# Kernel optimization log

Hardware: AMD Instinct MI355X
Metric: run time of the kernel (lower is better)

## Reference

```python
import jax, jax.numpy as jnp
import numpy as np

NUM_HEADS = 8


def _conv1x1(x, W, b):
    # 1x1 conv == per-pixel linear: x [N,C,H,W], W [O,C], b [O]
    return jnp.einsum('nchw,oc->nohw', x, W) + b[None, :, None, None]


def setup_inputs() -> dict:
    key = jax.random.key(0)
    ks = jax.random.split(key, 10)
    C = 512
    s = 1.0 / np.sqrt(C)  # keep pre-softmax logits in a sane range
    return {
        'x': jax.random.normal(ks[0], (2, C, 64, 64), dtype=jnp.float32),
        'Wq': jax.random.normal(ks[1], (C, C), dtype=jnp.float32) * s,
        'bq': jax.random.normal(ks[2], (C,), dtype=jnp.float32) * 0.01,
        'Wk': jax.random.normal(ks[3], (C, C), dtype=jnp.float32) * s,
        'bk': jax.random.normal(ks[4], (C,), dtype=jnp.float32) * 0.01,
        'Wv': jax.random.normal(ks[5], (C, C), dtype=jnp.float32) * s,
        'bv': jax.random.normal(ks[6], (C,), dtype=jnp.float32) * 0.01,
        'Wo': jax.random.normal(ks[7], (C, C), dtype=jnp.float32) * s,
        'bo': jax.random.normal(ks[8], (C,), dtype=jnp.float32) * 0.01,
        'gamma': jax.random.normal(ks[9], (1,), dtype=jnp.float32),
    }


def reference(x, Wq, bq, Wk, bk, Wv, bv, Wo, bo, gamma):
    N, C, H, W = x.shape
    nh = NUM_HEADS
    hd = C // nh
    S = H * W
    scale = 1.0 / (hd ** 0.5)
    # Projections via 1x1 conv, then split heads over flattened spatial tokens
    Q = _conv1x1(x, Wq, bq).reshape(N, nh, hd, S).transpose(0, 1, 3, 2)  # [N,h,S,d]
    K = _conv1x1(x, Wk, bk).reshape(N, nh, hd, S)                         # [N,h,d,S]
    V = _conv1x1(x, Wv, bv).reshape(N, nh, hd, S).transpose(0, 1, 3, 2)  # [N,h,S,d]
    attn = jax.nn.softmax(jnp.einsum('nhsd,nhdt->nhst', Q, K) * scale, axis=-1)
    out = jnp.einsum('nhst,nhtd->nhsd', attn, V)                          # [N,h,S,d]
    out = out.transpose(0, 1, 3, 2).reshape(N, C, H, W)
    out = _conv1x1(out, Wo, bo)
    return gamma[0] * out + x
```

## Files before the change

kernel.cpp:

```cpp
#include <hip/hip_runtime.h>
#include <hip/hip_bf16.h>

typedef __attribute__((ext_vector_type(4))) float f32x4;
typedef __attribute__((ext_vector_type(16))) float f32x16;
typedef __attribute__((ext_vector_type(8))) short s16x8;
typedef __attribute__((ext_vector_type(4))) unsigned short us16x4;
typedef __attribute__((ext_vector_type(4))) unsigned int u32x4;

#define C_DIM 512
#define S_DIM 4096
#define NB 2
#define NH 8
#define HD 64

#define QSCALE 0.1803368801111244f

__device__ __forceinline__ unsigned short f2bf(float f) {
    union { float f; unsigned u; } v; v.f = f;
    unsigned r = v.u + 0x7FFFu + ((v.u >> 16) & 1u);
    return (unsigned short)(r >> 16);
}

__device__ __forceinline__ float dev_exp2(float x) {
    float r;
    asm("v_exp_f32 %0, %1" : "=v"(r) : "v"(x));
    return r;
}

__device__ __forceinline__ unsigned cvt_pk_bf16(float lo, float hi) {
    unsigned r;
    asm("v_cvt_pk_bf16_f32 %0, %1, %2" : "=v"(r) : "v"(lo), "v"(hi));
    return r;
}

__device__ __forceinline__ void lane_swap(unsigned& a, unsigned& b) {
    asm("v_permlane32_swap_b32 %0, %1" : "+v"(a), "+v"(b));
}

__device__ __forceinline__ void gload_lds16(const void* g, void* l) {
    __builtin_amdgcn_global_load_lds(
        (const __attribute__((address_space(1))) void*)g,
        (__attribute__((address_space(3))) void*)l, 16, 0, 0);
}

__global__ __launch_bounds__(256) void wconv_kernel(
    const float* __restrict__ Wq, const float* __restrict__ Wk,
    const float* __restrict__ Wv, const float* __restrict__ Wo,
    unsigned short* __restrict__ Wb) {
    int i = blockIdx.x * 256 + threadIdx.x;
    int y = blockIdx.y;
    const float* src = (y == 0) ? Wq : (y == 1) ? Wk : (y == 2) ? Wv : Wo;
    Wb[(size_t)y * 262144 + i] = f2bf(src[i]);
}

__global__ __launch_bounds__(256) void xpose_kernel(
    const float* __restrict__ x, unsigned short* __restrict__ Xt) {
    __shared__ float tile[32][132];
    int n = blockIdx.z;
    int s0 = blockIdx.x * 128;
    int c0 = blockIdx.y * 32;
    int t = threadIdx.x;
    int cr = t >> 3, scol = (t & 7) * 16;
    const float* src = &x[((size_t)n * C_DIM + c0 + cr) * S_DIM + s0 + scol];
#pragma unroll
    for (int i = 0; i < 4; ++i)
        *(f32x4*)&tile[cr][scol + i * 4] = *(const f32x4*)&src[i * 4];
    __syncthreads();
    int sr = t >> 1, ch = (t & 1) * 16;
    unsigned short* dst = &Xt[((size_t)n * S_DIM + s0 + sr) * C_DIM + c0 + ch];
#pragma unroll
    for (int half = 0; half < 2; ++half) {
        s16x8 pk;
#pragma unroll
        for (int j = 0; j < 8; ++j)
            pk[j] = (short)f2bf(tile[ch + half * 8 + j][sr]);
        *(s16x8*)&dst[half * 8] = pk;
    }
}

__global__ __launch_bounds__(256) void qkv_gemm_kernel(
    const unsigned short* __restrict__ Wb, const unsigned short* __restrict__ Xt,
    const float* __restrict__ bq, const float* __restrict__ bk, const float* __restrict__ bv,
    unsigned short* __restrict__ Qt, unsigned short* __restrict__ Kt,
    unsigned short* __restrict__ Vb) {
    __shared__ unsigned short As[128 * 64];
    __shared__ unsigned short Bs[128 * 64];
    int w = blockIdx.z >> 1;
    int n = blockIdx.z & 1;
    const unsigned short* A = Wb + (size_t)w * 262144;
    const unsigned short* B = Xt + (size_t)n * S_DIM * C_DIM;
    int tid = threadIdx.x;
    int wid = tid >> 6, lane = tid & 63;
    int wm = wid >> 1, wn = wid & 1;
    int lr = lane & 15, lq = lane >> 4;
    int bm = blockIdx.y * 128, bt = blockIdx.x * 128;
    int r_in = lane >> 3, c8 = (lane & 7) * 8;

    f32x4 zero = {0.f, 0.f, 0.f, 0.f};
    f32x4 acc[4][4];
#pragma unroll
    for (int i = 0; i < 4; ++i)
#pragma unroll
        for (int j = 0; j < 4; ++j) acc[i][j] = zero;

    for (int ks = 0; ks < 8; ++ks) {
#pragma unroll
        for (int q = 0; q < 4; ++q) {
            int row = wid * 32 + q * 8;
            gload_lds16(A + (size_t)(bm + row + r_in) * C_DIM + ks * 64 + c8, &As[row * 64]);
            gload_lds16(B + (size_t)(bt + row + r_in) * C_DIM + ks * 64 + c8, &Bs[row * 64]);
        }
        __syncthreads();
#pragma unroll
        for (int kk = 0; kk < 2; ++kk) {
            s16x8 af[4], bf[4];
#pragma unroll
            for (int i = 0; i < 4; ++i)
                af[i] = *(const s16x8*)&As[(wm * 64 + i * 16 + lr) * 64 + kk * 32 + lq * 8];
#pragma unroll
            for (int j = 0; j < 4; ++j)
                bf[j] = *(const s16x8*)&Bs[(wn * 64 + j * 16 + lr) * 64 + kk * 32 + lq * 8];
#pragma unroll
            for (int i = 0; i < 4; ++i)
#pragma unroll
                for (int j = 0; j < 4; ++j)
                    acc[i][j] = __builtin_amdgcn_mfma_f32_16x16x32_bf16(af[i], bf[j], acc[i][j], 0, 0, 0);
        }
        __syncthreads();
    }

    const float* bias = (w == 0) ? bq : (w == 1) ? bk : bv;
#pragma unroll
    for (int i = 0; i < 4; ++i) {
        int obase = bm + wm * 64 + i * 16 + lq * 4;
#pragma unroll
        for (int j = 0; j < 4; ++j) {
            int t = bt + wn * 64 + j * 16 + lr;
            if (w == 0) {
                us16x4 pk;
#pragma unroll
                for (int r = 0; r < 4; ++r)
                    pk[r] = f2bf((acc[i][j][r] + bias[obase + r]) * QSCALE);
                int h = obase >> 6, d = obase & 63;
                *(us16x4*)&Qt[(((size_t)(n * NH + h) * S_DIM) + t) * HD + d] = pk;
            } else if (w == 1) {
                us16x4 pk;
#pragma unroll
                for (int r = 0; r < 4; ++r) pk[r] = f2bf(acc[i][j][r] + bias[obase + r]);
                int h = obase >> 6, d = obase & 63;
                *(us16x4*)&Kt[(((size_t)(n * NH + h) * S_DIM) + t) * HD + d] = pk;
            } else {
#pragma unroll
                for (int r = 0; r < 4; ++r) {
                    int o = obase + r;
                    Vb[((size_t)(n * C_DIM + o)) * S_DIM + t] = f2bf(acc[i][j][r] + bias[o]);
                }
            }
        }
    }
}

__global__ __launch_bounds__(256) void attn_kernel(
    const unsigned short* __restrict__ Qt, const unsigned short* __restrict__ Kt,
    const unsigned short* __restrict__ Vb, unsigned short* __restrict__ Ot) {
    __shared__ unsigned short Ks[64 * 64];
    __shared__ unsigned short Vs[64 * 64];
    int tid = threadIdx.x, wid = tid >> 6, lane = tid & 63;
    int l31 = lane & 31, hi = lane >> 5;
    int radj = (l31 & 7) ^ ((l31 >> 3) & 3);

    int bidl = blockIdx.x;
    int swz = (bidl & 7) * 64 + (bidl >> 3);
    int nh = swz >> 5;
    int qb = swz & 31;
    int n = nh >> 3, h = nh & 7;
    int qrow0 = qb * 128 + wid * 32;

    const unsigned short* Qh = Qt + (size_t)nh * S_DIM * HD;
    const unsigned short* Kh = Kt + (size_t)nh * S_DIM * HD;
    const unsigned short* Vh = Vb + ((size_t)(n * C_DIM + h * HD)) * S_DIM;

    s16x8 qf[4];
#pragma unroll
    for (int st = 0; st < 4; ++st)
        qf[st] = *(const s16x8*)&Qh[((size_t)(qrow0 + l31)) * HD + st * 16 + hi * 8];

    s16x8 ones;
#pragma unroll
    for (int r = 0; r < 8; ++r) ones[r] = (short)0x3F80;

    f32x16 Oacc[2], Lacc;
#pragma unroll
    for (int jm = 0; jm < 2; ++jm)
#pragma unroll
        for (int r = 0; r < 16; ++r) Oacc[jm][r] = 0.f;
#pragma unroll
    for (int r = 0; r < 16; ++r) Lacc[r] = 0.f;

    int srow0 = tid >> 3, sslot = tid & 7;
    int wslot = (sslot ^ (srow0 & 7) ^ ((srow0 >> 3) & 3)) * 8;

    s16x8 kreg[2], vreg[2];
#pragma unroll
    for (int q = 0; q < 2; ++q) {
        int row = srow0 + q * 32;
        kreg[q] = *(const s16x8*)&Kh[((size_t)row) * HD + sslot * 8];
        vreg[q] = *(const s16x8*)&Vh[((size_t)row) * S_DIM + sslot * 8];
    }

    for (int kt = 0; kt < 64; ++kt) {
#pragma unroll
        for (int q = 0; q < 2; ++q) {
            int row = srow0 + q * 32;
            *(s16x8*)&Ks[row * 64 + wslot] = kreg[q];
            *(s16x8*)&Vs[row * 64 + wslot] = vreg[q];
        }
        __syncthreads();
        if (kt < 63) {
#pragma unroll
            for (int q = 0; q < 2; ++q) {
                int row = srow0 + q * 32;
                kreg[q] = *(const s16x8*)&Kh[((size_t)((kt + 1) * 64 + row)) * HD + sslot * 8];
                vreg[q] = *(const s16x8*)&Vh[((size_t)row) * S_DIM + (kt + 1) * 64 + sslot * 8];
            }
        }

        f32x16 s_[2];
#pragma unroll
        for (int jm = 0; jm < 2; ++jm) {
#pragma unroll
            for (int r = 0; r < 16; ++r) s_[jm][r] = 0.f;
            int arow = jm * 32 + l31;
#pragma unroll
            for (int st = 0; st < 4; ++st) {
                s16x8 kf = *(const s16x8*)&Ks[arow * 64 + ((2 * st + hi) ^ radj) * 8];
                s_[jm] = __builtin_amdgcn_mfma_f32_32x32x16_bf16(kf, qf[st], s_[jm], 0, 0, 0);
            }
        }

        s16x8 pf[2][2];
#pragma unroll
        for (int jm = 0; jm < 2; ++jm) {
            unsigned pk0 = cvt_pk_bf16(dev_exp2(s_[jm][0]),  dev_exp2(s_[jm][1]));
            unsigned pk1 = cvt_pk_bf16(dev_exp2(s_[jm][2]),  dev_exp2(s_[jm][3]));
            unsigned pk2 = cvt_pk_bf16(dev_exp2(s_[jm][4]),  dev_exp2(s_[jm][5]));
            unsigned pk3 = cvt_pk_bf16(dev_exp2(s_[jm][6]),  dev_exp2(s_[jm][7]));
            unsigned pk4 = cvt_pk_bf16(dev_exp2(s_[jm][8]),  dev_exp2(s_[jm][9]));
            unsigned pk5 = cvt_pk_bf16(dev_exp2(s_[jm][10]), dev_exp2(s_[jm][11]));
            unsigned pk6 = cvt_pk_bf16(dev_exp2(s_[jm][12]), dev_exp2(s_[jm][13]));
            unsigned pk7 = cvt_pk_bf16(dev_exp2(s_[jm][14]), dev_exp2(s_[jm][15]));
            lane_swap(pk2, pk0);
            lane_swap(pk3, pk1);
            lane_swap(pk6, pk4);
            lane_swap(pk7, pk5);
            u32x4 w0 = {pk0, pk1, pk2, pk3};
            u32x4 w1 = {pk4, pk5, pk6, pk7};
            pf[jm][0] = __builtin_bit_cast(s16x8, w0);
            pf[jm][1] = __builtin_bit_cast(s16x8, w1);
        }

#pragma unroll
        for (int jm = 0; jm < 2; ++jm)
#pragma unroll
            for (int st = 0; st < 2; ++st)
                Lacc = __builtin_amdgcn_mfma_f32_32x32x16_bf16(ones, pf[jm][st], Lacc, 0, 0, 0);

#pragma unroll
        for (int jm2 = 0; jm2 < 2; ++jm2) {
            int vrow = jm2 * 32 + l31;
#pragma unroll
            for (int jm = 0; jm < 2; ++jm)
#pragma unroll
                for (int st = 0; st < 2; ++st) {
                    s16x8 vf = *(const s16x8*)&Vs[vrow * 64 + ((jm * 4 + st * 2 + hi) ^ radj) * 8];
                    Oacc[jm2] = __builtin_amdgcn_mfma_f32_32x32x16_bf16(vf, pf[jm][st], Oacc[jm2], 0, 0, 0);
                }
        }
        __syncthreads();
    }

    float inv = 1.f / Lacc[0];
    int token = qrow0 + l31;
    unsigned short* orow = Ot + ((size_t)n * S_DIM + token) * C_DIM + h * HD;
#pragma unroll
    for (int jm2 = 0; jm2 < 2; ++jm2)
#pragma unroll
        for (int rq = 0; rq < 4; ++rq) {
            int d = jm2 * 32 + 8 * rq + 4 * hi;
            us16x4 pk;
#pragma unroll
            for (int r = 0; r < 4; ++r) pk[r] = f2bf(Oacc[jm2][rq * 4 + r] * inv);
            *(us16x4*)&orow[d] = pk;
        }
}

__global__ __launch_bounds__(256) void out_gemm_kernel(
    const unsigned short* __restrict__ Wb, const unsigned short* __restrict__ Ot,
    const float* __restrict__ bo, const float* __restrict__ gamma,
    const float* __restrict__ xin, float* __restrict__ out) {
    __shared__ unsigned short As[128 * 64];
    __shared__ unsigned short Bs[128 * 64];
    int n = blockIdx.z;
    const unsigned short* A = Wb + (size_t)3 * 262144;
    const unsigned short* B = Ot + (size_t)n * S_DIM * C_DIM;
    int tid = threadIdx.x;
    int wid = tid >> 6, lane = tid & 63;
    int wm = wid >> 1, wn = wid & 1;
    int lr = lane & 15, lq = lane >> 4;
    int bm = blockIdx.y * 128, bt = blockIdx.x * 128;
    int r_in = lane >> 3, c8 = (lane & 7) * 8;

    f32x4 zero = {0.f, 0.f, 0.f, 0.f};
    f32x4 acc[4][4];
#pragma unroll
    for (int i = 0; i < 4; ++i)
#pragma unroll
        for (int j = 0; j < 4; ++j) acc[i][j] = zero;

    for (int ks = 0; ks < 8; ++ks) {
#pragma unroll
        for (int q = 0; q < 4; ++q) {
            int row = wid * 32 + q * 8;
            gload_lds16(A + (size_t)(bm + row + r_in) * C_DIM + ks * 64 + c8, &As[row * 64]);
            gload_lds16(B + (size_t)(bt + row + r_in) * C_DIM + ks * 64 + c8, &Bs[row * 64]);
        }
        __syncthreads();
#pragma unroll
        for (int kk = 0; kk < 2; ++kk) {
            s16x8 af[4], bf[4];
#pragma unroll
            for (int i = 0; i < 4; ++i)
                af[i] = *(const s16x8*)&As[(wm * 64 + i * 16 + lr) * 64 + kk * 32 + lq * 8];
#pragma unroll
            for (int j = 0; j < 4; ++j)
                bf[j] = *(const s16x8*)&Bs[(wn * 64 + j * 16 + lr) * 64 + kk * 32 + lq * 8];
#pragma unroll
            for (int i = 0; i < 4; ++i)
#pragma unroll
                for (int j = 0; j < 4; ++j)
                    acc[i][j] = __builtin_amdgcn_mfma_f32_16x16x32_bf16(af[i], bf[j], acc[i][j], 0, 0, 0);
        }
        __syncthreads();
    }

    float g = gamma[0];
#pragma unroll
    for (int i = 0; i < 4; ++i) {
        int obase = bm + wm * 64 + i * 16 + lq * 4;
#pragma unroll
        for (int j = 0; j < 4; ++j) {
            int t = bt + wn * 64 + j * 16 + lr;
#pragma unroll
            for (int r = 0; r < 4; ++r) {
                int o = obase + r;
                size_t idx = ((size_t)(n * C_DIM + o)) * S_DIM + t;
                out[idx] = g * (acc[i][j][r] + bo[o]) + xin[idx];
            }
        }
    }
}

extern "C" void kernel_launch(void* const* d_in, const int* in_sizes, int n_in,
                              void* d_out, int out_size, void* d_ws, size_t ws_size,
                              hipStream_t stream) {
    const float* x  = (const float*)d_in[0];
    const float* Wq = (const float*)d_in[1];
    const float* bq = (const float*)d_in[2];
    const float* Wk = (const float*)d_in[3];
    const float* bk = (const float*)d_in[4];
    const float* Wv = (const float*)d_in[5];
    const float* bv = (const float*)d_in[6];
    const float* Wo = (const float*)d_in[7];
    const float* bo = (const float*)d_in[8];
    const float* gamma = (const float*)d_in[9];
    float* out = (float*)d_out;

    char* ws = (char*)d_ws;
    unsigned short* Wb = (unsigned short*)ws;
    unsigned short* Xt = (unsigned short*)(ws + ((size_t)2  << 20));
    unsigned short* Qt = (unsigned short*)(ws + ((size_t)10 << 20));
    unsigned short* Kt = (unsigned short*)(ws + ((size_t)18 << 20));
    unsigned short* Vb = (unsigned short*)(ws + ((size_t)26 << 20));
    unsigned short* Ot = (unsigned short*)(ws + ((size_t)34 << 20));

    wconv_kernel<<<dim3(1024, 4), 256, 0, stream>>>(Wq, Wk, Wv, Wo, Wb);
    xpose_kernel<<<dim3(32, 16, 2), 256, 0, stream>>>(x, Xt);
    qkv_gemm_kernel<<<dim3(32, 4, 6), 256, 0, stream>>>(Wb, Xt, bq, bk, bv, Qt, Kt, Vb);
    attn_kernel<<<512, 256, 0, stream>>>(Qt, Kt, Vb, Ot);
    out_gemm_kernel<<<dim3(32, 4, 2), 256, 0, stream>>>(Wb, Ot, bo, gamma, x, out);
}
```

Measured before the change: 147.1 us.

## Double-buffer K/V tiles in attention with direct global-to-LDS loads

The attention kernel previously prefetched the next K/V tile into registers and then wrote it to a single shared-memory buffer, with barriers around each write. It now keeps two LDS buffers per tensor and issues direct global-to-LDS loads for tile kt+1 while computing on tile kt. The XOR swizzle moves from the LDS write address to the global source address. This is meant to remove the register staging and ds_write traffic and to overlap loads with MFMA work. In exchange it doubles LDS use per block, which can lower occupancy, and it relies on the barrier correctly waiting for the async LDS loads.

```diff
diff --git a/kernel.cpp b/kernel.cpp
--- a/kernel.cpp
+++ b/kernel.cpp
@@ -163,8 +163,8 @@
 __global__ __launch_bounds__(256) void attn_kernel(
     const unsigned short* __restrict__ Qt, const unsigned short* __restrict__ Kt,
     const unsigned short* __restrict__ Vb, unsigned short* __restrict__ Ot) {
-    __shared__ unsigned short Ks[64 * 64];
-    __shared__ unsigned short Vs[64 * 64];
+    __shared__ unsigned short Ks[2][64 * 64];
+    __shared__ unsigned short Vs[2][64 * 64];
     int tid = threadIdx.x, wid = tid >> 6, lane = tid & 63;
     int l31 = lane & 31, hi = lane >> 5;
     int radj = (l31 & 7) ^ ((l31 >> 3) & 3);
@@ -197,33 +197,29 @@
 #pragma unroll
     for (int r = 0; r < 16; ++r) Lacc[r] = 0.f;
 
-    int srow0 = tid >> 3, sslot = tid & 7;
-    int wslot = (sslot ^ (srow0 & 7) ^ ((srow0 >> 3) & 3)) * 8;
-
-    s16x8 kreg[2], vreg[2];
-#pragma unroll
-    for (int q = 0; q < 2; ++q) {
-        int row = srow0 + q * 32;
-        kreg[q] = *(const s16x8*)&Kh[((size_t)row) * HD + sslot * 8];
-        vreg[q] = *(const s16x8*)&Vh[((size_t)row) * S_DIM + sslot * 8];
-    }
+    int lr8 = lane >> 3, pslot = lane & 7;
+    int row_a = wid * 16 + lr8;
+    int row_b = row_a + 8;
+    int sca = (pslot ^ (row_a & 7) ^ ((row_a >> 3) & 3)) * 8;
+    int scb = (pslot ^ (row_b & 7) ^ ((row_b >> 3) & 3)) * 8;
+    int rb_a = (wid * 16) * 64;
+    int rb_b = (wid * 16 + 8) * 64;
+
+#define STAGE_KV(buf, kt_) {                                                        \
+        const unsigned short* kb_ = Kh + ((size_t)((kt_) * 64)) * HD;               \
+        gload_lds16(kb_ + (size_t)row_a * HD + sca, &Ks[buf][rb_a]);                \
+        gload_lds16(kb_ + (size_t)row_b * HD + scb, &Ks[buf][rb_b]);                \
+        const unsigned short* vb_ = Vh + (kt_) * 64;                                \
+        gload_lds16(vb_ + (size_t)row_a * S_DIM + sca, &Vs[buf][rb_a]);             \
+        gload_lds16(vb_ + (size_t)row_b * S_DIM + scb, &Vs[buf][rb_b]);             \
+    }
+
+    STAGE_KV(0, 0);
+    __syncthreads();
 
     for (int kt = 0; kt < 64; ++kt) {
-#pragma unroll
-        for (int q = 0; q < 2; ++q) {
-            int row = srow0 + q * 32;
-            *(s16x8*)&Ks[row * 64 + wslot] = kreg[q];
-            *(s16x8*)&Vs[row * 64 + wslot] = vreg[q];
-        }
-        __syncthreads();
-        if (kt < 63) {
-#pragma unroll
-            for (int q = 0; q < 2; ++q) {
-                int row = srow0 + q * 32;
-                kreg[q] = *(const s16x8*)&Kh[((size_t)((kt + 1) * 64 + row)) * HD + sslot * 8];
-                vreg[q] = *(const s16x8*)&Vh[((size_t)row) * S_DIM + (kt + 1) * 64 + sslot * 8];
-            }
-        }
+        int cur = kt & 1;
+        if (kt < 63) STAGE_KV(cur ^ 1, kt + 1);
 
         f32x16 s_[2];
 #pragma unroll
@@ -233,7 +229,7 @@
             int arow = jm * 32 + l31;
 #pragma unroll
             for (int st = 0; st < 4; ++st) {
-                s16x8 kf = *(const s16x8*)&Ks[arow * 64 + ((2 * st + hi) ^ radj) * 8];
+                s16x8 kf = *(const s16x8*)&Ks[cur][arow * 64 + ((2 * st + hi) ^ radj) * 8];
                 s_[jm] = __builtin_amdgcn_mfma_f32_32x32x16_bf16(kf, qf[st], s_[jm], 0, 0, 0);
             }
         }
@@ -272,12 +268,14 @@
             for (int jm = 0; jm < 2; ++jm)
 #pragma unroll
                 for (int st = 0; st < 2; ++st) {
-                    s16x8 vf = *(const s16x8*)&Vs[vrow * 64 + ((jm * 4 + st * 2 + hi) ^ radj) * 8];
+                    s16x8 vf = *(const s16x8*)&Vs[cur][vrow * 64 + ((jm * 4 + st * 2 + hi) ^ radj) * 8];
                     Oacc[jm2] = __builtin_amdgcn_mfma_f32_32x32x16_bf16(vf, pf[jm][st], Oacc[jm2], 0, 0, 0);
                 }
         }
-        __syncthreads();
-    }
+
+        __syncthreads();
+    }
+#undef STAGE_KV
 
     float inv = 1.f / Lacc[0];
     int token = qrow0 + l31;
```

Result: slower. 158.2 us (+7.5%).

## Process two K/V tiles per iteration in attention kernel

Applied to the files above, without the earlier changes.

The attention loop now stages two 64-token K/V tiles in shared memory per iteration and computes both score blocks and PV updates together, halving the number of loop iterations and barrier pairs. Global prefetch loads twice as much data ahead, giving more independent MFMA and exp work per barrier to hide latency. It doubles LDS use and raises register pressure (two score accumulators, two P fragments, four prefetch registers), which may reduce occupancy.

```diff
diff --git a/kernel.cpp b/kernel.cpp
--- a/kernel.cpp
+++ b/kernel.cpp
@@ -163,8 +163,8 @@
 __global__ __launch_bounds__(256) void attn_kernel(
     const unsigned short* __restrict__ Qt, const unsigned short* __restrict__ Kt,
     const unsigned short* __restrict__ Vb, unsigned short* __restrict__ Ot) {
-    __shared__ unsigned short Ks[64 * 64];
-    __shared__ unsigned short Vs[64 * 64];
+    __shared__ unsigned short Ks[2][64 * 64];
+    __shared__ unsigned short Vs[2][64 * 64];
     int tid = threadIdx.x, wid = tid >> 6, lane = tid & 63;
     int l31 = lane & 31, hi = lane >> 5;
     int radj = (l31 & 7) ^ ((l31 >> 3) & 3);
@@ -200,70 +200,92 @@
     int srow0 = tid >> 3, sslot = tid & 7;
     int wslot = (sslot ^ (srow0 & 7) ^ ((srow0 >> 3) & 3)) * 8;
 
-    s16x8 kreg[2], vreg[2];
+    s16x8 kA[2], vA[2], kB[2], vB[2];
 #pragma unroll
     for (int q = 0; q < 2; ++q) {
         int row = srow0 + q * 32;
-        kreg[q] = *(const s16x8*)&Kh[((size_t)row) * HD + sslot * 8];
-        vreg[q] = *(const s16x8*)&Vh[((size_t)row) * S_DIM + sslot * 8];
-    }
-
-    for (int kt = 0; kt < 64; ++kt) {
-#pragma unroll
-        for (int q = 0; q < 2; ++q) {
-            int row = srow0 + q * 32;
-            *(s16x8*)&Ks[row * 64 + wslot] = kreg[q];
-            *(s16x8*)&Vs[row * 64 + wslot] = vreg[q];
-        }
-        __syncthreads();
-        if (kt < 63) {
+        kA[q] = *(const s16x8*)&Kh[((size_t)row) * HD + sslot * 8];
+        vA[q] = *(const s16x8*)&Vh[((size_t)row) * S_DIM + sslot * 8];
+        kB[q] = *(const s16x8*)&Kh[((size_t)(64 + row)) * HD + sslot * 8];
+        vB[q] = *(const s16x8*)&Vh[((size_t)row) * S_DIM + 64 + sslot * 8];
+    }
+#pragma unroll
+    for (int q = 0; q < 2; ++q) {
+        int row = srow0 + q * 32;
+        *(s16x8*)&Ks[0][row * 64 + wslot] = kA[q];
+        *(s16x8*)&Vs[0][row * 64 + wslot] = vA[q];
+        *(s16x8*)&Ks[1][row * 64 + wslot] = kB[q];
+        *(s16x8*)&Vs[1][row * 64 + wslot] = vB[q];
+    }
+    __syncthreads();
+
+    for (int kt = 0; kt < 64; kt += 2) {
+        if (kt < 62) {
 #pragma unroll
             for (int q = 0; q < 2; ++q) {
                 int row = srow0 + q * 32;
-                kreg[q] = *(const s16x8*)&Kh[((size_t)((kt + 1) * 64 + row)) * HD + sslot * 8];
-                vreg[q] = *(const s16x8*)&Vh[((size_t)row) * S_DIM + (kt + 1) * 64 + sslot * 8];
-            }
-        }
-
-        f32x16 s_[2];
+                kA[q] = *(const s16x8*)&Kh[((size_t)((kt + 2) * 64 + row)) * HD + sslot * 8];
+                vA[q] = *(const s16x8*)&Vh[((size_t)row) * S_DIM + (kt + 2) * 64 + sslot * 8];
+                kB[q] = *(const s16x8*)&Kh[((size_t)((kt + 3) * 64 + row)) * HD + sslot * 8];
+                vB[q] = *(const s16x8*)&Vh[((size_t)row) * S_DIM + (kt + 3) * 64 + sslot * 8];
+            }
+        }
+
+        f32x16 sA[2], sB[2];
 #pragma unroll
         for (int jm = 0; jm < 2; ++jm) {
 #pragma unroll
-            for (int r = 0; r < 16; ++r) s_[jm][r] = 0.f;
+            for (int r = 0; r < 16; ++r) { sA[jm][r] = 0.f; sB[jm][r] = 0.f; }
             int arow = jm * 32 + l31;
 #pragma unroll
             for (int st = 0; st < 4; ++st) {
-                s16x8 kf = *(const s16x8*)&Ks[arow * 64 + ((2 * st + hi) ^ radj) * 8];
-                s_[jm] = __builtin_amdgcn_mfma_f32_32x32x16_bf16(kf, qf[st], s_[jm], 0, 0, 0);
-            }
-        }
-
-        s16x8 pf[2][2];
+                int slot = ((2 * st + hi) ^ radj) * 8;
+                s16x8 kfA = *(const s16x8*)&Ks[0][arow * 64 + slot];
+                s16x8 kfB = *(const s16x8*)&Ks[1][arow * 64 + slot];
+                sA[jm] = __builtin_amdgcn_mfma_f32_32x32x16_bf16(kfA, qf[st], sA[jm], 0, 0, 0);
+                sB[jm] = __builtin_amdgcn_mfma_f32_32x32x16_bf16(kfB, qf[st], sB[jm], 0, 0, 0);
+            }
+        }
+
+        s16x8 pfA[2][2], pfB[2][2];
 #pragma unroll
         for (int jm = 0; jm < 2; ++jm) {
-            unsigned pk0 = cvt_pk_bf16(dev_exp2(s_[jm][0]),  dev_exp2(s_[jm][1]));
-            unsigned pk1 = cvt_pk_bf16(dev_exp2(s_[jm][2]),  dev_exp2(s_[jm][3]));
-            unsigned pk2 = cvt_pk_bf16(dev_exp2(s_[jm][4]),  dev_exp2(s_[jm][5]));
-            unsigned pk3 = cvt_pk_bf16(dev_exp2(s_[jm][6]),  dev_exp2(s_[jm][7]));
-            unsigned pk4 = cvt_pk_bf16(dev_exp2(s_[jm][8]),  dev_exp2(s_[jm][9]));
-            unsigned pk5 = cvt_pk_bf16(dev_exp2(s_[jm][10]), dev_exp2(s_[jm][11]));
-            unsigned pk6 = cvt_pk_bf16(dev_exp2(s_[jm][12]), dev_exp2(s_[jm][13]));
-            unsigned pk7 = cvt_pk_bf16(dev_exp2(s_[jm][14]), dev_exp2(s_[jm][15]));
-            lane_swap(pk2, pk0);
-            lane_swap(pk3, pk1);
-            lane_swap(pk6, pk4);
-            lane_swap(pk7, pk5);
-            u32x4 w0 = {pk0, pk1, pk2, pk3};
-            u32x4 w1 = {pk4, pk5, pk6, pk7};
-            pf[jm][0] = __builtin_bit_cast(s16x8, w0);
-            pf[jm][1] = __builtin_bit_cast(s16x8, w1);
+            unsigned a0 = cvt_pk_bf16(dev_exp2(sA[jm][0]),  dev_exp2(sA[jm][1]));
+            unsigned a1 = cvt_pk_bf16(dev_exp2(sA[jm][2]),  dev_exp2(sA[jm][3]));
+            unsigned a2 = cvt_pk_bf16(dev_exp2(sA[jm][4]),  dev_exp2(sA[jm][5]));
+            unsigned a3 = cvt_pk_bf16(dev_exp2(sA[jm][6]),  dev_exp2(sA[jm][7]));
+            unsigned a4 = cvt_pk_bf16(dev_exp2(sA[jm][8]),  dev_exp2(sA[jm][9]));
+            unsigned a5 = cvt_pk_bf16(dev_exp2(sA[jm][10]), dev_exp2(sA[jm][11]));
+            unsigned a6 = cvt_pk_bf16(dev_exp2(sA[jm][12]), dev_exp2(sA[jm][13]));
+            unsigned a7 = cvt_pk_bf16(dev_exp2(sA[jm][14]), dev_exp2(sA[jm][15]));
+            lane_swap(a2, a0); lane_swap(a3, a1); lane_swap(a6, a4); lane_swap(a7, a5);
+            u32x4 wa0 = {a0, a1, a2, a3};
+            u32x4 wa1 = {a4, a5, a6, a7};
+            pfA[jm][0] = __builtin_bit_cast(s16x8, wa0);
+            pfA[jm][1] = __builtin_bit_cast(s16x8, wa1);
+
+            unsigned b0 = cvt_pk_bf16(dev_exp2(sB[jm][0]),  dev_exp2(sB[jm][1]));
+            unsigned b1 = cvt_pk_bf16(dev_exp2(sB[jm][2]),  dev_exp2(sB[jm][3]));
+            unsigned b2 = cvt_pk_bf16(dev_exp2(sB[jm][4]),  dev_exp2(sB[jm][5]));
+            unsigned b3 = cvt_pk_bf16(dev_exp2(sB[jm][6]),  dev_exp2(sB[jm][7]));
+            unsigned b4 = cvt_pk_bf16(dev_exp2(sB[jm][8]),  dev_exp2(sB[jm][9]));
+            unsigned b5 = cvt_pk_bf16(dev_exp2(sB[jm][10]), dev_exp2(sB[jm][11]));
+            unsigned b6 = cvt_pk_bf16(dev_exp2(sB[jm][12]), dev_exp2(sB[jm][13]));
+            unsigned b7 = cvt_pk_bf16(dev_exp2(sB[jm][14]), dev_exp2(sB[jm][15]));
+            lane_swap(b2, b0); lane_swap(b3, b1); lane_swap(b6, b4); lane_swap(b7, b5);
+            u32x4 wb0 = {b0, b1, b2, b3};
+            u32x4 wb1 = {b4, b5, b6, b7};
+            pfB[jm][0] = __builtin_bit_cast(s16x8, wb0);
+            pfB[jm][1] = __builtin_bit_cast(s16x8, wb1);
         }
 
 #pragma unroll
         for (int jm = 0; jm < 2; ++jm)
 #pragma unroll
-            for (int st = 0; st < 2; ++st)
-                Lacc = __builtin_amdgcn_mfma_f32_32x32x16_bf16(ones, pf[jm][st], Lacc, 0, 0, 0);
+            for (int st = 0; st < 2; ++st) {
+                Lacc = __builtin_amdgcn_mfma_f32_32x32x16_bf16(ones, pfA[jm][st], Lacc, 0, 0, 0);
+                Lacc = __builtin_amdgcn_mfma_f32_32x32x16_bf16(ones, pfB[jm][st], Lacc, 0, 0, 0);
+            }
 
 #pragma unroll
         for (int jm2 = 0; jm2 < 2; ++jm2) {
@@ -272,11 +294,26 @@
             for (int jm = 0; jm < 2; ++jm)
 #pragma unroll
                 for (int st = 0; st < 2; ++st) {
-                    s16x8 vf = *(const s16x8*)&Vs[vrow * 64 + ((jm * 4 + st * 2 + hi) ^ radj) * 8];
-                    Oacc[jm2] = __builtin_amdgcn_mfma_f32_32x32x16_bf16(vf, pf[jm][st], Oacc[jm2], 0, 0, 0);
+                    int slot = ((jm * 4 + st * 2 + hi) ^ radj) * 8;
+                    s16x8 vfA = *(const s16x8*)&Vs[0][vrow * 64 + slot];
+                    s16x8 vfB = *(const s16x8*)&Vs[1][vrow * 64 + slot];
+                    Oacc[jm2] = __builtin_amdgcn_mfma_f32_32x32x16_bf16(vfA, pfA[jm][st], Oacc[jm2], 0, 0, 0);
+                    Oacc[jm2] = __builtin_amdgcn_mfma_f32_32x32x16_bf16(vfB, pfB[jm][st], Oacc[jm2], 0, 0, 0);
                 }
         }
         __syncthreads();
+
+        if (kt < 62) {
+#pragma unroll
+            for (int q = 0; q < 2; ++q) {
+                int row = srow0 + q * 32;
+                *(s16x8*)&Ks[0][row * 64 + wslot] = kA[q];
+                *(s16x8*)&Vs[0][row * 64 + wslot] = vA[q];
+                *(s16x8*)&Ks[1][row * 64 + wslot] = kB[q];
+                *(s16x8*)&Vs[1][row * 64 + wslot] = vB[q];
+            }
+            __syncthreads();
+        }
     }
 
     float inv = 1.f / Lacc[0];
```

After: 160.9 us. 9.3% more time.
